# Optimization experiments

Measured on AMD Instinct MI355X. Metric: run time of the kernel, lower is better.

## Reference

```python
import jax, jax.numpy as jnp
import numpy as np

B, S, D = 4, 2048, 1024
NEG_INF = jnp.float32(-jnp.inf)


def setup_inputs() -> dict:
    key = jax.random.key(0)
    kx, kq, kk, kv = jax.random.split(key, 4)
    scale = 0.02
    return {
        "x": jax.random.normal(kx, (B, S, D), dtype=jnp.float32),
        "Wq": jax.random.normal(kq, (D, D), dtype=jnp.float32) * scale,
        "Wk": jax.random.normal(kk, (D, D), dtype=jnp.float32) * scale,
        "Wv": jax.random.normal(kv, (D, D), dtype=jnp.float32) * scale,
    }


def reference(x, Wq, Wk, Wv):
    # nn.Linear(d_in, d_out): y = x @ W.T (no bias; qkv_bias=False)
    q = jnp.einsum("bsd,ed->bse", x, Wq)
    k = jnp.einsum("bsd,ed->bse", x, Wk)
    v = jnp.einsum("bsd,ed->bse", x, Wv)
    n = x.shape[1]
    scores = jnp.einsum("bqe,bke->bqk", q, k)  # [B, S, S]
    # causal mask: positions k > q are masked with -inf
    causal = jnp.tril(jnp.ones((n, n), dtype=bool))
    scores = jnp.where(causal[None, :, :], scores, NEG_INF)
    attn = jax.nn.softmax(scores / jnp.sqrt(jnp.float32(k.shape[-1])), axis=-1)
    # dropout p=0.0 (eval) -> identity
    return jnp.einsum("bqk,bke->bqe", attn, v)
```

## Files before the change

kernel.cpp:

```cpp
#include <hip/hip_runtime.h>
#include <hip/hip_bf16.h>
#include <stdint.h>
#include <stddef.h>


typedef __hip_bfloat16 bf16;
typedef short short8 __attribute__((ext_vector_type(8)));
typedef short short4v __attribute__((ext_vector_type(4)));
typedef float f32x4 __attribute__((ext_vector_type(4)));

#define BM 128
#define BN 128
#define BK 64
#define MSZ 8192
#define DD 1024

__device__ __forceinline__ void cstore(float* p, float v) { *p = v; }
__device__ __forceinline__ void cstore(bf16* p, float v) { *p = __float2bfloat16(v); }

__global__ __launch_bounds__(256)
void f2b(const float* __restrict__ s, bf16* __restrict__ d, int n) {
  const int i = (blockIdx.x * 256 + threadIdx.x) * 4;
  if (i >= n) return;
  const float4 v = *(const float4*)(s + i);
  bf16 t[4] = {__float2bfloat16(v.x), __float2bfloat16(v.y),
               __float2bfloat16(v.z), __float2bfloat16(v.w)};
  *(short4v*)(d + i) = *(short4v*)t;
}

__global__ __launch_bounds__(256)
void f2b3(const float* __restrict__ a, const float* __restrict__ b,
          const float* __restrict__ c, bf16* __restrict__ d, int n) {
  const float* s = (blockIdx.y == 0) ? a : (blockIdx.y == 1) ? b : c;
  const int i = (blockIdx.x * 256 + threadIdx.x) * 4;
  if (i >= n) return;
  const float4 v = *(const float4*)(s + i);
  bf16 t[4] = {__float2bfloat16(v.x), __float2bfloat16(v.y),
               __float2bfloat16(v.z), __float2bfloat16(v.w)};
  *(short4v*)(d + (size_t)blockIdx.y * n + i) = *(short4v*)t;
}

__global__ __launch_bounds__(512, 1)
void qkv_8p(const bf16* __restrict__ A, const bf16* __restrict__ B,
            bf16* __restrict__ C, bf16* __restrict__ C2) {
  __shared__ short8 As[2][2048];
  __shared__ short8 Bs[2][1024];

  const int flat = blockIdx.x;
  const int c = flat & 7, j = flat >> 3;
  const int by = c * 4 + (j & 3), bx = j >> 2;
  const int bm0 = by * 256, bn0 = bx * 128;
  const int tid = threadIdx.x, wave = tid >> 6, lane = tid & 63;
  const int wm = wave >> 1, wn = wave & 1;
  const int l15 = lane & 15, q4 = lane >> 4;
  const int rh = l15 >> 3, r3 = l15 & 7;
  const int sr = lane & 7, sgk = (lane >> 3) & 3, shb = lane >> 5;

  const bf16* apg = A + (size_t)(bm0 + wave * 32 + shb * 8 + sr) * DD + sgk * 8;
  const bf16* bpg = B + (size_t)(bn0 + wave * 16 + shb * 8 + sr) * DD + sgk * 8;

  const int NT = DD / 64;

  auto stage = [&](int t, int ks) {
    const int b = t & 1;
    const size_t ko = (size_t)(t * 64 + ks * 32);
#pragma unroll
    for (int i = 0; i < 2; i++)
      __builtin_amdgcn_global_load_lds(apg + (size_t)(i * 16) * DD + ko,
                                       &As[b][ks * 1024 + wave * 128 + i * 64], 16, 0, 0);
    __builtin_amdgcn_global_load_lds(bpg + ko,
                                     &Bs[b][ks * 512 + wave * 64], 16, 0, 0);
  };

  const int fa = wm * 256 + rh * 32 + q4 * 8 + r3;
  const int fb = wn * 256 + rh * 32 + q4 * 8 + r3;

  f32x4 acc[4][4] = {};

  stage(0, 0);
  stage(0, 1);
  asm volatile("s_waitcnt vmcnt(3)" ::: "memory");
  asm volatile("s_barrier" ::: "memory");

  for (int t = 0; t < NT; ++t) {
    const int b = t & 1;
#pragma unroll
    for (int ks = 0; ks < 2; ++ks) {
      short8 af[4], bfr[4];
#pragma unroll
      for (int i = 0; i < 4; i++) af[i] = As[b][ks * 1024 + fa + i * 64];
#pragma unroll
      for (int jj = 0; jj < 4; jj++) bfr[jj] = Bs[b][ks * 512 + fb + jj * 64];
      if (t + 1 < NT) {
        stage(t + 1, ks);
        asm volatile("s_waitcnt vmcnt(3)" ::: "memory");
      } else {
        asm volatile("s_waitcnt vmcnt(0)" ::: "memory");
      }
      asm volatile("s_barrier" ::: "memory");
      __builtin_amdgcn_s_setprio(1);
#pragma unroll
      for (int i = 0; i < 4; i++)
#pragma unroll
        for (int jj = 0; jj < 4; jj++)
          acc[i][jj] = __builtin_amdgcn_mfma_f32_16x16x32_bf16(af[i], bfr[jj], acc[i][jj], 0, 0, 0);
      __builtin_amdgcn_s_setprio(0);
      asm volatile("s_barrier" ::: "memory");
    }
  }

  if (bx >= 16) {
#pragma unroll
    for (int i = 0; i < 4; i++) {
#pragma unroll
      for (int jj = 0; jj < 4; jj++) {
        const int rowb = bm0 + wm * 64 + i * 16 + q4 * 4;
        const int v = (bn0 - 2048) + wn * 64 + jj * 16 + l15;
        bf16 t4[4] = {__float2bfloat16(acc[i][jj][0]), __float2bfloat16(acc[i][jj][1]),
                      __float2bfloat16(acc[i][jj][2]), __float2bfloat16(acc[i][jj][3])};
        *(short4v*)(C2 + (size_t)v * MSZ + rowb) = *(short4v*)t4;
      }
    }
    return;
  }
  bf16* Cb = C + (bx >= 8 ? (size_t)MSZ * DD : 0);
  const int coff = (bx & 7) * 128;
#pragma unroll
  for (int i = 0; i < 4; i++) {
#pragma unroll
    for (int jj = 0; jj < 4; jj++) {
#pragma unroll
      for (int r = 0; r < 4; r++) {
        const int row = bm0 + wm * 64 + i * 16 + q4 * 4 + r;
        const int col = coff + wn * 64 + jj * 16 + l15;
        Cb[(size_t)row * DD + col] = __float2bfloat16(acc[i][jj][r]);
      }
    }
  }
}

template <int MODE, typename CT>
__global__ __launch_bounds__(256, 4)
void gemm_bt(const bf16* __restrict__ A, const bf16* __restrict__ B,
             CT* __restrict__ C, bf16* __restrict__ C2,
             int lda, int ldb, int ldc, int K,
             long sA, long sB, long sC, float scale) {
  int by, bx, zb;
  const int flat = blockIdx.x;
  const int c = flat & 7, j = flat >> 3;
  if (MODE == 2) {
    zb = c >> 1;
    const int t = (c & 1) * 68 + j;
    by = (int)((__fsqrt_rn(8.f * (float)t + 1.f) - 1.f) * 0.5f);
    while ((by + 1) * (by + 2) / 2 <= t) by++;
    while (by * (by + 1) / 2 > t) by--;
    bx = t - by * (by + 1) / 2;
  } else {
    zb = c >> 1;
    bx = j & 7;
    by = 2 * (7 - (j >> 3)) + (c & 1);
  }

  __shared__ short8 As[1024];
  __shared__ short8 Bs[1024];

  const int tid = threadIdx.x;
  const int wave = tid >> 6, lane = tid & 63;
  const int wm = wave >> 1, wn = wave & 1;
  const int l15 = lane & 15, q4 = lane >> 4;
  const int bm0 = by * BM, bn0 = bx * BN;

  const bf16* Az = A + (long)zb * sA;
  const bf16* Bz = B + (long)zb * sB;
  CT* Cz = C + (long)zb * sC;

  const int sg = lane >> 3, sr = lane & 7;
  const bf16* apg = Az + (size_t)(bm0 + wave * 32 + sr) * lda + sg * 8;
  const bf16* bpg = Bz + (size_t)(bn0 + wave * 32 + sr) * ldb + sg * 8;
  short8* asw = &As[wave * 256];
  short8* bsw = &Bs[wave * 256];

  const int Ke = (MODE == 3) ? min(K, (by + 1) * BM) : K;

  const int rh = l15 >> 3, r3 = l15 & 7;
  const int fra = wm * 512 + rh * 64 + q4 * 8 + r3;
  const int frb = wn * 512 + rh * 64 + q4 * 8 + r3;

  f32x4 acc[4][4] = {};

  for (int k0 = 0; k0 < Ke; k0 += BK) {
#pragma unroll
    for (int jj = 0; jj < 4; jj++) {
      __builtin_amdgcn_global_load_lds(apg + (size_t)jj * 8 * lda + k0,
                                       asw + jj * 64, 16, 0, 0);
      __builtin_amdgcn_global_load_lds(bpg + (size_t)jj * 8 * ldb + k0,
                                       bsw + jj * 64, 16, 0, 0);
    }
    __syncthreads();

#pragma unroll
    for (int s = 0; s < 2; s++) {
      short8 af[4], bfr[4];
#pragma unroll
      for (int i = 0; i < 4; i++) af[i] = As[fra + i * 128 + s * 32];
#pragma unroll
      for (int jj = 0; jj < 4; jj++) bfr[jj] = Bs[frb + jj * 128 + s * 32];
#pragma unroll
      for (int i = 0; i < 4; i++)
#pragma unroll
        for (int jj = 0; jj < 4; jj++)
          acc[i][jj] = __builtin_amdgcn_mfma_f32_16x16x32_bf16(af[i], bfr[jj], acc[i][jj], 0, 0, 0);
    }
    __syncthreads();
  }

#pragma unroll
  for (int i = 0; i < 4; i++) {
#pragma unroll
    for (int jj = 0; jj < 4; jj++) {
#pragma unroll
      for (int r = 0; r < 4; r++) {
        const int row = bm0 + wm * 64 + i * 16 + q4 * 4 + r;
        const int col = bn0 + wn * 64 + jj * 16 + l15;
        cstore(&Cz[(size_t)row * ldc + col], acc[i][jj][r] * scale);
      }
    }
  }
}

__global__ __launch_bounds__(256)
void softmax_rows(const bf16* __restrict__ Sc, bf16* __restrict__ P, int S) {
  const int q = blockIdx.x, b = blockIdx.y;
  const short8* srow = (const short8*)(Sc + ((size_t)b * S + q) * S);
  short8* prow = (short8*)(P + ((size_t)b * S + q) * S);
  const int len = q + 1;
  const int tid = threadIdx.x;
  const int wave = tid >> 6, lane = tid & 63;
  __shared__ float red[10];

  const short8 raw = srow[tid];
  float v[8];
#pragma unroll
  for (int j = 0; j < 8; j++) {
    const int k = tid * 8 + j;
    const float f = __bfloat162float(((const bf16*)&raw)[j]);
    v[j] = (k < len) ? f : -1e30f;
  }

  float m = v[0];
#pragma unroll
  for (int j = 1; j < 8; j++) m = fmaxf(m, v[j]);
#pragma unroll
  for (int o = 32; o; o >>= 1) m = fmaxf(m, __shfl_down(m, o));
  if (lane == 0) red[wave] = m;
  __syncthreads();
  if (tid == 0) red[8] = fmaxf(fmaxf(red[0], red[1]), fmaxf(red[2], red[3]));
  __syncthreads();
  const float M = red[8];

  float e[8], s = 0.f;
#pragma unroll
  for (int j = 0; j < 8; j++) { e[j] = __expf(v[j] - M); s += e[j]; }
#pragma unroll
  for (int o = 32; o; o >>= 1) s += __shfl_down(s, o);
  if (lane == 0) red[4 + wave] = s;
  __syncthreads();
  if (tid == 0) red[9] = red[4] + red[5] + red[6] + red[7];
  __syncthreads();
  const float inv = 1.f / red[9];

  short8 outp;
#pragma unroll
  for (int j = 0; j < 8; j++) {
    const int k = tid * 8 + j;
    ((bf16*)&outp)[j] = __float2bfloat16((k < len) ? e[j] * inv : 0.f);
  }
  prow[tid] = outp;
}

extern "C" void kernel_launch(void* const* d_in, const int* in_sizes, int n_in,
                              void* d_out, int out_size, void* d_ws, size_t ws_size,
                              hipStream_t stream) {
  const float* x  = (const float*)d_in[0];
  const float* Wq = (const float*)d_in[1];
  const float* Wk = (const float*)d_in[2];
  const float* Wv = (const float*)d_in[3];
  float* out = (float*)d_out;

  const int Bb = 4, S = 2048, D = 1024, MS = Bb * S;

  char* ws = (char*)d_ws;
  bf16* xb = (bf16*)ws;
  bf16* wb = (bf16*)(ws + (size_t)MS * D * 2);
  bf16* Q  = (bf16*)(ws + (size_t)MS * D * 2 + 3u * D * D * 2);
  bf16* Kp = Q + (size_t)MS * D;
  bf16* VT = Kp + (size_t)MS * D;
  bf16* Sc = VT + (size_t)MS * D;
  bf16* P  = (bf16*)ws;
  (void)Kp;

  dim3 blk(256);

  f2b<<<dim3(MS * D / 4 / 256), blk, 0, stream>>>(x, xb, MS * D);
  f2b3<<<dim3(D * D / 4 / 256, 3), blk, 0, stream>>>(Wq, Wk, Wv, wb, D * D);

  qkv_8p<<<dim3(768), dim3(512), 0, stream>>>(xb, wb, Q, VT);
  gemm_bt<2, bf16><<<dim3(544), blk, 0, stream>>>(
      Q, Kp, Sc, nullptr, D, D, S, D,
      (long)S * D, (long)S * D, (long)S * S, 0.03125f);
  softmax_rows<<<dim3(S, Bb), blk, 0, stream>>>(Sc, P, S);
  gemm_bt<3, float><<<dim3(512), blk, 0, stream>>>(
      P, VT, out, nullptr, S, MS, D, S,
      (long)S * S, (long)S, (long)S * D, 1.f);
}
```

Measured before the change: 292.3 us.

## Double-buffer score and PV GEMMs with split-K staging and larger score tiles

Replaces the generic gemm_bt template with two specialized kernels. Both double-buffer their LDS tiles and stage the next K-slice while MFMAs run, using explicit vmcnt waits, barriers and setprio in place of two full __syncthreads per iteration. The score kernel also moves to 256x128 tiles with 512 threads and a new triangular block mapping of 288 blocks. The extra LDS and larger tiles lower occupancy, and the hand-written waitcnt logic is fragile.

```diff
diff --git a/kernel.cpp b/kernel.cpp
--- a/kernel.cpp
+++ b/kernel.cpp
@@ -9,14 +9,9 @@
 typedef short short4v __attribute__((ext_vector_type(4)));
 typedef float f32x4 __attribute__((ext_vector_type(4)));
 
-#define BM 128
-#define BN 128
-#define BK 64
 #define MSZ 8192
 #define DD 1024
-
-__device__ __forceinline__ void cstore(float* p, float v) { *p = v; }
-__device__ __forceinline__ void cstore(bf16* p, float v) { *p = __float2bfloat16(v); }
+#define SS 2048
 
 __global__ __launch_bounds__(256)
 void f2b(const float* __restrict__ s, bf16* __restrict__ d, int n) {
@@ -139,81 +134,84 @@
   }
 }
 
-template <int MODE, typename CT>
-__global__ __launch_bounds__(256, 4)
-void gemm_bt(const bf16* __restrict__ A, const bf16* __restrict__ B,
-             CT* __restrict__ C, bf16* __restrict__ C2,
-             int lda, int ldb, int ldc, int K,
-             long sA, long sB, long sC, float scale) {
-  int by, bx, zb;
+__global__ __launch_bounds__(512, 1)
+void sc_dp(const bf16* __restrict__ Q, const bf16* __restrict__ Kp,
+           bf16* __restrict__ Sc) {
+  __shared__ short8 As[2][2048];
+  __shared__ short8 Bs[2][1024];
+
   const int flat = blockIdx.x;
-  const int c = flat & 7, j = flat >> 3;
-  if (MODE == 2) {
-    zb = c >> 1;
-    const int t = (c & 1) * 68 + j;
-    by = (int)((__fsqrt_rn(8.f * (float)t + 1.f) - 1.f) * 0.5f);
-    while ((by + 1) * (by + 2) / 2 <= t) by++;
-    while (by * (by + 1) / 2 > t) by--;
-    bx = t - by * (by + 1) / 2;
-  } else {
-    zb = c >> 1;
-    bx = j & 7;
-    by = 2 * (7 - (j >> 3)) + (c & 1);
-  }
-
-  __shared__ short8 As[1024];
-  __shared__ short8 Bs[1024];
-
-  const int tid = threadIdx.x;
-  const int wave = tid >> 6, lane = tid & 63;
+  const int c = flat & 7;
+  const int zb = c >> 1;
+  const int t = (c & 1) * 36 + (flat >> 3);
+  int by = (int)((__fsqrt_rn(4.f * (float)t + 1.f) - 1.f) * 0.5f);
+  while ((by + 1) * (by + 2) <= t) by++;
+  while (by * (by + 1) > t) by--;
+  const int bx = t - by * (by + 1);
+
+  const int bm0 = by * 256, bn0 = bx * 128;
+  const int tid = threadIdx.x, wave = tid >> 6, lane = tid & 63;
   const int wm = wave >> 1, wn = wave & 1;
   const int l15 = lane & 15, q4 = lane >> 4;
-  const int bm0 = by * BM, bn0 = bx * BN;
-
-  const bf16* Az = A + (long)zb * sA;
-  const bf16* Bz = B + (long)zb * sB;
-  CT* Cz = C + (long)zb * sC;
-
-  const int sg = lane >> 3, sr = lane & 7;
-  const bf16* apg = Az + (size_t)(bm0 + wave * 32 + sr) * lda + sg * 8;
-  const bf16* bpg = Bz + (size_t)(bn0 + wave * 32 + sr) * ldb + sg * 8;
-  short8* asw = &As[wave * 256];
-  short8* bsw = &Bs[wave * 256];
-
-  const int Ke = (MODE == 3) ? min(K, (by + 1) * BM) : K;
-
   const int rh = l15 >> 3, r3 = l15 & 7;
-  const int fra = wm * 512 + rh * 64 + q4 * 8 + r3;
-  const int frb = wn * 512 + rh * 64 + q4 * 8 + r3;
+  const int sr = lane & 7, sgk = (lane >> 3) & 3, shb = lane >> 5;
+
+  const bf16* Az = Q + (size_t)zb * SS * DD;
+  const bf16* Bz = Kp + (size_t)zb * SS * DD;
+  const bf16* apg = Az + (size_t)(bm0 + wave * 32 + shb * 8 + sr) * DD + sgk * 8;
+  const bf16* bpg = Bz + (size_t)(bn0 + wave * 16 + shb * 8 + sr) * DD + sgk * 8;
+
+  const int NT = DD / 64;
+
+  auto stage = [&](int tt, int ks) {
+    const int b = tt & 1;
+    const size_t ko = (size_t)(tt * 64 + ks * 32);
+#pragma unroll
+    for (int i = 0; i < 2; i++)
+      __builtin_amdgcn_global_load_lds(apg + (size_t)(i * 16) * DD + ko,
+                                       &As[b][ks * 1024 + wave * 128 + i * 64], 16, 0, 0);
+    __builtin_amdgcn_global_load_lds(bpg + ko,
+                                     &Bs[b][ks * 512 + wave * 64], 16, 0, 0);
+  };
+
+  const int fa = wm * 256 + rh * 32 + q4 * 8 + r3;
+  const int fb = wn * 256 + rh * 32 + q4 * 8 + r3;
 
   f32x4 acc[4][4] = {};
 
-  for (int k0 = 0; k0 < Ke; k0 += BK) {
-#pragma unroll
-    for (int jj = 0; jj < 4; jj++) {
-      __builtin_amdgcn_global_load_lds(apg + (size_t)jj * 8 * lda + k0,
-                                       asw + jj * 64, 16, 0, 0);
-      __builtin_amdgcn_global_load_lds(bpg + (size_t)jj * 8 * ldb + k0,
-                                       bsw + jj * 64, 16, 0, 0);
-    }
-    __syncthreads();
-
-#pragma unroll
-    for (int s = 0; s < 2; s++) {
+  stage(0, 0);
+  stage(0, 1);
+  asm volatile("s_waitcnt vmcnt(3)" ::: "memory");
+  asm volatile("s_barrier" ::: "memory");
+
+  for (int tt = 0; tt < NT; ++tt) {
+    const int b = tt & 1;
+#pragma unroll
+    for (int ks = 0; ks < 2; ++ks) {
       short8 af[4], bfr[4];
 #pragma unroll
-      for (int i = 0; i < 4; i++) af[i] = As[fra + i * 128 + s * 32];
-#pragma unroll
-      for (int jj = 0; jj < 4; jj++) bfr[jj] = Bs[frb + jj * 128 + s * 32];
+      for (int i = 0; i < 4; i++) af[i] = As[b][ks * 1024 + fa + i * 64];
+#pragma unroll
+      for (int jj = 0; jj < 4; jj++) bfr[jj] = Bs[b][ks * 512 + fb + jj * 64];
+      if (tt + 1 < NT) {
+        stage(tt + 1, ks);
+        asm volatile("s_waitcnt vmcnt(3)" ::: "memory");
+      } else {
+        asm volatile("s_waitcnt vmcnt(0)" ::: "memory");
+      }
+      asm volatile("s_barrier" ::: "memory");
+      __builtin_amdgcn_s_setprio(1);
 #pragma unroll
       for (int i = 0; i < 4; i++)
 #pragma unroll
         for (int jj = 0; jj < 4; jj++)
           acc[i][jj] = __builtin_amdgcn_mfma_f32_16x16x32_bf16(af[i], bfr[jj], acc[i][jj], 0, 0, 0);
-    }
-    __syncthreads();
-  }
-
+      __builtin_amdgcn_s_setprio(0);
+      asm volatile("s_barrier" ::: "memory");
+    }
+  }
+
+  bf16* Cz = Sc + (size_t)zb * SS * SS;
 #pragma unroll
   for (int i = 0; i < 4; i++) {
 #pragma unroll
@@ -222,7 +220,98 @@
       for (int r = 0; r < 4; r++) {
         const int row = bm0 + wm * 64 + i * 16 + q4 * 4 + r;
         const int col = bn0 + wn * 64 + jj * 16 + l15;
-        cstore(&Cz[(size_t)row * ldc + col], acc[i][jj][r] * scale);
+        Cz[(size_t)row * SS + col] = __float2bfloat16(acc[i][jj][r] * 0.03125f);
+      }
+    }
+  }
+}
+
+__global__ __launch_bounds__(256, 2)
+void pv_dp(const bf16* __restrict__ P, const bf16* __restrict__ VT,
+           float* __restrict__ out) {
+  __shared__ short8 As[2][1024];
+  __shared__ short8 Bs[2][1024];
+
+  const int flat = blockIdx.x;
+  const int c = flat & 7, j = flat >> 3;
+  const int zb = c >> 1;
+  const int bx = j & 7;
+  const int by = 2 * (7 - (j >> 3)) + (c & 1);
+
+  const int bm0 = by * 128, bn0 = bx * 128;
+  const int tid = threadIdx.x, wave = tid >> 6, lane = tid & 63;
+  const int wm = wave >> 1, wn = wave & 1;
+  const int l15 = lane & 15, q4 = lane >> 4;
+  const int rh = l15 >> 3, r3 = l15 & 7;
+  const int sr = lane & 7, sgk = (lane >> 3) & 3, shb = lane >> 5;
+
+  const bf16* Az = P + (size_t)zb * SS * SS;
+  const bf16* Bz = VT + (size_t)zb * SS;
+  const bf16* apg = Az + (size_t)(bm0 + wave * 32 + shb * 8 + sr) * SS + sgk * 8;
+  const bf16* bpg = Bz + (size_t)(bn0 + wave * 32 + shb * 8 + sr) * MSZ + sgk * 8;
+
+  const int Ke = min(SS, (by + 1) * 128);
+  const int NT = Ke >> 6;
+
+  auto stage = [&](int t, int ks) {
+    const int b = t & 1;
+    const size_t ko = (size_t)(t * 64 + ks * 32);
+#pragma unroll
+    for (int i = 0; i < 2; i++) {
+      __builtin_amdgcn_global_load_lds(apg + (size_t)(i * 16) * SS + ko,
+                                       &As[b][ks * 512 + wave * 128 + i * 64], 16, 0, 0);
+      __builtin_amdgcn_global_load_lds(bpg + (size_t)(i * 16) * MSZ + ko,
+                                       &Bs[b][ks * 512 + wave * 128 + i * 64], 16, 0, 0);
+    }
+  };
+
+  const int fa = wm * 256 + rh * 32 + q4 * 8 + r3;
+  const int fb = wn * 256 + rh * 32 + q4 * 8 + r3;
+
+  f32x4 acc[4][4] = {};
+
+  stage(0, 0);
+  stage(0, 1);
+  asm volatile("s_waitcnt vmcnt(4)" ::: "memory");
+  asm volatile("s_barrier" ::: "memory");
+
+  for (int t = 0; t < NT; ++t) {
+    const int b = t & 1;
+#pragma unroll
+    for (int ks = 0; ks < 2; ++ks) {
+      short8 af[4], bfr[4];
+#pragma unroll
+      for (int i = 0; i < 4; i++) af[i] = As[b][ks * 512 + fa + i * 64];
+#pragma unroll
+      for (int jj = 0; jj < 4; jj++) bfr[jj] = Bs[b][ks * 512 + fb + jj * 64];
+      if (t + 1 < NT) {
+        stage(t + 1, ks);
+        asm volatile("s_waitcnt vmcnt(4)" ::: "memory");
+      } else {
+        asm volatile("s_waitcnt vmcnt(0)" ::: "memory");
+      }
+      asm volatile("s_barrier" ::: "memory");
+      __builtin_amdgcn_s_setprio(1);
+#pragma unroll
+      for (int i = 0; i < 4; i++)
+#pragma unroll
+        for (int jj = 0; jj < 4; jj++)
+          acc[i][jj] = __builtin_amdgcn_mfma_f32_16x16x32_bf16(af[i], bfr[jj], acc[i][jj], 0, 0, 0);
+      __builtin_amdgcn_s_setprio(0);
+      asm volatile("s_barrier" ::: "memory");
+    }
+  }
+
+  float* Cz = out + (size_t)zb * SS * DD;
+#pragma unroll
+  for (int i = 0; i < 4; i++) {
+#pragma unroll
+    for (int jj = 0; jj < 4; jj++) {
+#pragma unroll
+      for (int r = 0; r < 4; r++) {
+        const int row = bm0 + wm * 64 + i * 16 + q4 * 4 + r;
+        const int col = bn0 + wn * 64 + jj * 16 + l15;
+        Cz[(size_t)row * DD + col] = acc[i][jj][r];
       }
     }
   }
@@ -305,11 +394,7 @@
   f2b3<<<dim3(D * D / 4 / 256, 3), blk, 0, stream>>>(Wq, Wk, Wv, wb, D * D);
 
   qkv_8p<<<dim3(768), dim3(512), 0, stream>>>(xb, wb, Q, VT);
-  gemm_bt<2, bf16><<<dim3(544), blk, 0, stream>>>(
-      Q, Kp, Sc, nullptr, D, D, S, D,
-      (long)S * D, (long)S * D, (long)S * S, 0.03125f);
+  sc_dp<<<dim3(288), dim3(512), 0, stream>>>(Q, Kp, Sc);
   softmax_rows<<<dim3(S, Bb), blk, 0, stream>>>(Sc, P, S);
-  gemm_bt<3, float><<<dim3(512), blk, 0, stream>>>(
-      P, VT, out, nullptr, S, MS, D, S,
-      (long)S * S, (long)S, (long)S * D, 1.f);
-}
+  pv_dp<<<dim3(512), blk, 0, stream>>>(P, VT, out);
+}
```

Result: faster. 285.2 us (-2.4%).
